# Performance work log

Hardware: AMD Instinct MI355X
Metric: run time of the kernel (lower is better)

The kernel has to match this reference:

```python
import jax, jax.numpy as jnp
import numpy as np

B, H, N, P = 2, 8, 2048, 64   # batch, heads, seq, head_dim
M, D = 4, 256                 # sketch count, sketch feature dim


def setup_inputs() -> dict:
    key = jax.random.key(0)
    kq, kk, ks, kr = jax.random.split(key, 4)
    scale = P ** -0.5  # keep exp(QK) numerically tame, std(dot) ~= 1/8
    Q = jax.random.normal(kq, (B, H, N, P), dtype=jnp.float32) * scale
    K = jax.random.normal(kk, (B, H, N, P), dtype=jnp.float32) * scale
    # indices into the concatenated [Q;K] token axis of length 2N
    sketching_matrix = jax.random.randint(ks, (B, M, D), 0, 2 * N)
    # Rademacher random signs, broadcast over [b,h,2n] in the reduction
    random_sign = jnp.sign(jax.random.normal(kr, (M, D), dtype=jnp.float32))
    random_sign = jnp.where(random_sign == 0, 1.0, random_sign)
    return {"Q": Q, "K": K, "sketching_matrix": sketching_matrix,
            "random_sign": random_sign}


def reference(Q, K, sketching_matrix, random_sign):
    b, h, n, p = Q.shape
    X = jnp.concatenate([Q, K], axis=2)          # [b,h,2n,p]
    Xt = jnp.transpose(X, (0, 2, 1, 3))          # [b,2n,h,p]
    # gather sketched landmarks: [b,m,d,h,p] -> [b,h,m,d,p]
    XS = Xt[jnp.arange(b)[:, None, None], sketching_matrix]
    XS = jnp.transpose(XS, (0, 3, 1, 2, 4))
    # RS_SM accumulate branch: exp of inner products, random-sign reduce over m
    product = jnp.einsum('bhnp,bhmdp->bhnmd', X, XS)   # [b,h,2n,m,d]
    AS = jnp.einsum('bhnmd,md->bhnd', jnp.exp(product), random_sign)
    return AS.astype(Q.dtype)                    # [b,h,2n,d]
```

## Files before the change

### kernel.cpp

```cpp
#include <hip/hip_runtime.h>
#include <hip/hip_bf16.h>

typedef __attribute__((ext_vector_type(8))) short short8;
typedef __attribute__((ext_vector_type(4))) float f32x4;

namespace {
constexpr int Nc  = 2048;
constexpr int NXc = 4096;
constexpr int Pc  = 64;
constexpr int Mc  = 4;
constexpr int Dc  = 256;
constexpr int BH  = 16;
constexpr int LDW = 72;
constexpr float LOG2E = 1.4426950408889634f;
}

__device__ inline float fexp2(float x) {
#if __has_builtin(__builtin_amdgcn_exp2f)
  return __builtin_amdgcn_exp2f(x);
#else
  return exp2f(x);
#endif
}

__device__ inline unsigned int bfpack(float a, float b) {
  union { __hip_bfloat162 h; unsigned int u; } cv;
  cv.h = __float22bfloat162_rn(make_float2(a, b));
  return cv.u;
}

__global__ __launch_bounds__(256) void prepass_kernel(
    const float* __restrict__ Q, const float* __restrict__ K,
    const int* __restrict__ SK, __hip_bfloat16* __restrict__ Wb)
{
  const int t  = blockIdx.x * 256 + threadIdx.x;
  const int q  = t & 7;
  const int r  = t >> 3;
  const int bh = r >> 10;
  const int md = r & 1023;
  const int b  = bh >> 3;
  const int idx = SK[b * (Mc * Dc) + md];
  const float* src = (idx < Nc) ? (Q + ((size_t)bh * Nc + idx) * Pc)
                                : (K + ((size_t)bh * Nc + (idx - Nc)) * Pc);
  const f32x4* s4 = (const f32x4*)(src + q * 8);
  f32x4 f0 = s4[0], f1 = s4[1];
  uint4 u;
  u.x = bfpack(f0.x * LOG2E, f0.y * LOG2E);
  u.y = bfpack(f0.z * LOG2E, f0.w * LOG2E);
  u.z = bfpack(f1.x * LOG2E, f1.y * LOG2E);
  u.w = bfpack(f1.z * LOG2E, f1.w * LOG2E);
  *(uint4*)(Wb + (size_t)r * Pc + q * 8) = u;
}

__global__ __launch_bounds__(256, 4) void sketch_main(
    const float* __restrict__ Q, const float* __restrict__ K,
    const __hip_bfloat16* __restrict__ Wb,
    const float* __restrict__ SGN, float* __restrict__ OUT)
{
  __shared__ __hip_bfloat16 Ws[2][64][LDW];
  __shared__ float Ss[Mc * Dc];

  const int t    = threadIdx.x;
  const int lane = t & 63;
  const int wv   = t >> 6;
  const int brow = lane & 15;
  const int q    = lane >> 4;
  const int bh   = blockIdx.y;
  const int n0   = blockIdx.x * 64;

  for (int i = t; i < Mc * Dc; i += 256) Ss[i] = SGN[i];

  const int nrow = n0 + wv * 16 + brow;
  const float* xsrc = (n0 < Nc) ? (Q + ((size_t)bh * Nc + nrow) * Pc)
                                : (K + ((size_t)bh * Nc + (nrow - Nc)) * Pc);
  f32x4 x0 = *(const f32x4*)(xsrc + q * 8);
  f32x4 x1 = *(const f32x4*)(xsrc + q * 8 + 4);
  f32x4 x2 = *(const f32x4*)(xsrc + 32 + q * 8);
  f32x4 x3 = *(const f32x4*)(xsrc + 32 + q * 8 + 4);
  short8 bfr0, bfr1;
  {
    union { short8 s; uint4 u; } c0, c1;
    c0.u.x = bfpack(x0.x, x0.y); c0.u.y = bfpack(x0.z, x0.w);
    c0.u.z = bfpack(x1.x, x1.y); c0.u.w = bfpack(x1.z, x1.w);
    c1.u.x = bfpack(x2.x, x2.y); c1.u.y = bfpack(x2.z, x2.w);
    c1.u.z = bfpack(x3.x, x3.y); c1.u.w = bfpack(x3.z, x3.w);
    bfr0 = c0.s; bfr1 = c1.s;
  }

  const __hip_bfloat16* wbase = Wb + (size_t)bh * (Mc * Dc) * Pc;
  const int tr = t >> 2;
  const int tq = t & 3;

  auto crow = [](int p) { return (p & 3) * Dc + (p >> 2) * 64; };

  {
    const __hip_bfloat16* wp = wbase + (size_t)(crow(0) + tr) * Pc + tq * 16;
    uint4 wa = *(const uint4*)wp;
    uint4 wb = *(const uint4*)(wp + 8);
    *(uint4*)&Ws[0][tr][tq * 16]     = wa;
    *(uint4*)&Ws[0][tr][tq * 16 + 8] = wb;
  }
  __syncthreads();

  f32x4 AS[4];
  #pragma unroll
  for (int dt = 0; dt < 4; ++dt) AS[dt] = (f32x4){0.f, 0.f, 0.f, 0.f};

  for (int p = 0; p < 16; ++p) {
    const int pn = (p < 15) ? p + 1 : 15;
    const __hip_bfloat16* wp = wbase + (size_t)(crow(pn) + tr) * Pc + tq * 16;
    uint4 wa = *(const uint4*)wp;
    uint4 wb = *(const uint4*)(wp + 8);

    const int buf = p & 1;
    const int m   = p & 3;
    const int dc  = p >> 2;

    #pragma unroll
    for (int dt = 0; dt < 4; ++dt) {
      short8 a0 = *(const short8*)&Ws[buf][dt * 16 + brow][q * 8];
      short8 a1 = *(const short8*)&Ws[buf][dt * 16 + brow][32 + q * 8];
      f32x4 c = {0.f, 0.f, 0.f, 0.f};
      c = __builtin_amdgcn_mfma_f32_16x16x32_bf16(a0, bfr0, c, 0, 0, 0);
      c = __builtin_amdgcn_mfma_f32_16x16x32_bf16(a1, bfr1, c, 0, 0, 0);
      const f32x4 sg = *(const f32x4*)&Ss[m * Dc + dc * 64 + dt * 16 + q * 4];
      AS[dt].x = fmaf(sg.x, fexp2(c.x), AS[dt].x);
      AS[dt].y = fmaf(sg.y, fexp2(c.y), AS[dt].y);
      AS[dt].z = fmaf(sg.z, fexp2(c.z), AS[dt].z);
      AS[dt].w = fmaf(sg.w, fexp2(c.w), AS[dt].w);
    }

    if (m == 3) {
      float* orow = OUT + ((size_t)bh * NXc + nrow) * Dc + dc * 64 + q * 4;
      #pragma unroll
      for (int dt = 0; dt < 4; ++dt) {
        *(f32x4*)(orow + dt * 16) = AS[dt];
        AS[dt] = (f32x4){0.f, 0.f, 0.f, 0.f};
      }
    }

    *(uint4*)&Ws[buf ^ 1][tr][tq * 16]     = wa;
    *(uint4*)&Ws[buf ^ 1][tr][tq * 16 + 8] = wb;
    __syncthreads();
  }
}

extern "C" void kernel_launch(void* const* d_in, const int* in_sizes, int n_in,
                              void* d_out, int out_size, void* d_ws, size_t ws_size,
                              hipStream_t stream) {
  (void)in_sizes; (void)n_in; (void)out_size; (void)ws_size;
  const float* Q   = (const float*)d_in[0];
  const float* K   = (const float*)d_in[1];
  const int*   SK  = (const int*)d_in[2];
  const float* SGN = (const float*)d_in[3];
  float* OUT = (float*)d_out;

  __hip_bfloat16* Wb = (__hip_bfloat16*)d_ws;

  prepass_kernel<<<dim3(512), dim3(256), 0, stream>>>(Q, K, SK, Wb);
  sketch_main<<<dim3(NXc / 64, BH), dim3(256), 0, stream>>>(Q, K, Wb, SGN, OUT);
}
```

Measured before the change: 102.2 us.

## Enlarge token tile to 128 and split sketch columns across waves

Each block now handles 128 tokens instead of 64. Each wave holds eight 16-token X fragments in registers and owns a fixed 16-column slice of the sketch landmarks. This reuses each LDS-loaded landmark fragment across eight MFMA tiles, cutting LDS reads and halving how often the shared landmark tile is reloaded from global memory per token. In exchange it raises register pressure (occupancy hint drops from 4 to 2 blocks), halves the number of blocks, and changes output stores to a strided row pattern.

```diff
diff --git a/kernel.cpp b/kernel.cpp
--- a/kernel.cpp
+++ b/kernel.cpp
@@ -11,6 +11,7 @@
 constexpr int Mc  = 4;
 constexpr int Dc  = 256;
 constexpr int BH  = 16;
+constexpr int TN  = 128;
 constexpr int LDW = 72;
 constexpr float LOG2E = 1.4426950408889634f;
 }
@@ -52,7 +53,7 @@
   *(uint4*)(Wb + (size_t)r * Pc + q * 8) = u;
 }
 
-__global__ __launch_bounds__(256, 4) void sketch_main(
+__global__ __launch_bounds__(256, 2) void sketch_main(
     const float* __restrict__ Q, const float* __restrict__ K,
     const __hip_bfloat16* __restrict__ Wb,
     const float* __restrict__ SGN, float* __restrict__ OUT)
@@ -66,25 +67,28 @@
   const int brow = lane & 15;
   const int q    = lane >> 4;
   const int bh   = blockIdx.y;
-  const int n0   = blockIdx.x * 64;
+  const int n0   = blockIdx.x * TN;
 
   for (int i = t; i < Mc * Dc; i += 256) Ss[i] = SGN[i];
 
-  const int nrow = n0 + wv * 16 + brow;
-  const float* xsrc = (n0 < Nc) ? (Q + ((size_t)bh * Nc + nrow) * Pc)
-                                : (K + ((size_t)bh * Nc + (nrow - Nc)) * Pc);
-  f32x4 x0 = *(const f32x4*)(xsrc + q * 8);
-  f32x4 x1 = *(const f32x4*)(xsrc + q * 8 + 4);
-  f32x4 x2 = *(const f32x4*)(xsrc + 32 + q * 8);
-  f32x4 x3 = *(const f32x4*)(xsrc + 32 + q * 8 + 4);
-  short8 bfr0, bfr1;
+  short8 bx[8][2];
   {
-    union { short8 s; uint4 u; } c0, c1;
-    c0.u.x = bfpack(x0.x, x0.y); c0.u.y = bfpack(x0.z, x0.w);
-    c0.u.z = bfpack(x1.x, x1.y); c0.u.w = bfpack(x1.z, x1.w);
-    c1.u.x = bfpack(x2.x, x2.y); c1.u.y = bfpack(x2.z, x2.w);
-    c1.u.z = bfpack(x3.x, x3.y); c1.u.w = bfpack(x3.z, x3.w);
-    bfr0 = c0.s; bfr1 = c1.s;
+    const float* xbase = (n0 < Nc) ? (Q + ((size_t)bh * Nc + n0) * Pc)
+                                   : (K + ((size_t)bh * Nc + (n0 - Nc)) * Pc);
+    #pragma unroll
+    for (int tj = 0; tj < 8; ++tj) {
+      const float* xr = xbase + (size_t)(tj * 16 + brow) * Pc + q * 8;
+      f32x4 f0 = *(const f32x4*)xr;
+      f32x4 f1 = *(const f32x4*)(xr + 4);
+      f32x4 f2 = *(const f32x4*)(xr + 32);
+      f32x4 f3 = *(const f32x4*)(xr + 36);
+      union { short8 s; uint4 u; } c0, c1;
+      c0.u.x = bfpack(f0.x, f0.y); c0.u.y = bfpack(f0.z, f0.w);
+      c0.u.z = bfpack(f1.x, f1.y); c0.u.w = bfpack(f1.z, f1.w);
+      c1.u.x = bfpack(f2.x, f2.y); c1.u.y = bfpack(f2.z, f2.w);
+      c1.u.z = bfpack(f3.x, f3.y); c1.u.w = bfpack(f3.z, f3.w);
+      bx[tj][0] = c0.s; bx[tj][1] = c1.s;
+    }
   }
 
   const __hip_bfloat16* wbase = Wb + (size_t)bh * (Mc * Dc) * Pc;
@@ -102,9 +106,9 @@
   }
   __syncthreads();
 
-  f32x4 AS[4];
+  f32x4 AS[8];
   #pragma unroll
-  for (int dt = 0; dt < 4; ++dt) AS[dt] = (f32x4){0.f, 0.f, 0.f, 0.f};
+  for (int tj = 0; tj < 8; ++tj) AS[tj] = (f32x4){0.f, 0.f, 0.f, 0.f};
 
   for (int p = 0; p < 16; ++p) {
     const int pn = (p < 15) ? p + 1 : 15;
@@ -116,26 +120,28 @@
     const int m   = p & 3;
     const int dc  = p >> 2;
 
+    short8 a0 = *(const short8*)&Ws[buf][wv * 16 + brow][q * 8];
+    short8 a1 = *(const short8*)&Ws[buf][wv * 16 + brow][32 + q * 8];
+
+    const f32x4 sg = *(const f32x4*)&Ss[m * Dc + dc * 64 + wv * 16 + q * 4];
+
     #pragma unroll
-    for (int dt = 0; dt < 4; ++dt) {
-      short8 a0 = *(const short8*)&Ws[buf][dt * 16 + brow][q * 8];
-      short8 a1 = *(const short8*)&Ws[buf][dt * 16 + brow][32 + q * 8];
+    for (int tj = 0; tj < 8; ++tj) {
       f32x4 c = {0.f, 0.f, 0.f, 0.f};
-      c = __builtin_amdgcn_mfma_f32_16x16x32_bf16(a0, bfr0, c, 0, 0, 0);
-      c = __builtin_amdgcn_mfma_f32_16x16x32_bf16(a1, bfr1, c, 0, 0, 0);
-      const f32x4 sg = *(const f32x4*)&Ss[m * Dc + dc * 64 + dt * 16 + q * 4];
-      AS[dt].x = fmaf(sg.x, fexp2(c.x), AS[dt].x);
-      AS[dt].y = fmaf(sg.y, fexp2(c.y), AS[dt].y);
-      AS[dt].z = fmaf(sg.z, fexp2(c.z), AS[dt].z);
-      AS[dt].w = fmaf(sg.w, fexp2(c.w), AS[dt].w);
+      c = __builtin_amdgcn_mfma_f32_16x16x32_bf16(a0, bx[tj][0], c, 0, 0, 0);
+      c = __builtin_amdgcn_mfma_f32_16x16x32_bf16(a1, bx[tj][1], c, 0, 0, 0);
+      AS[tj].x = fmaf(sg.x, fexp2(c.x), AS[tj].x);
+      AS[tj].y = fmaf(sg.y, fexp2(c.y), AS[tj].y);
+      AS[tj].z = fmaf(sg.z, fexp2(c.z), AS[tj].z);
+      AS[tj].w = fmaf(sg.w, fexp2(c.w), AS[tj].w);
     }
 
     if (m == 3) {
-      float* orow = OUT + ((size_t)bh * NXc + nrow) * Dc + dc * 64 + q * 4;
+      float* obase = OUT + ((size_t)bh * NXc + n0) * Dc + dc * 64 + wv * 16 + q * 4;
       #pragma unroll
-      for (int dt = 0; dt < 4; ++dt) {
-        *(f32x4*)(orow + dt * 16) = AS[dt];
-        AS[dt] = (f32x4){0.f, 0.f, 0.f, 0.f};
+      for (int tj = 0; tj < 8; ++tj) {
+        *(f32x4*)(obase + (size_t)(tj * 16 + brow) * Dc) = AS[tj];
+        AS[tj] = (f32x4){0.f, 0.f, 0.f, 0.f};
       }
     }
 
@@ -158,5 +164,5 @@
   __hip_bfloat16* Wb = (__hip_bfloat16*)d_ws;
 
   prepass_kernel<<<dim3(512), dim3(256), 0, stream>>>(Q, K, SK, Wb);
-  sketch_main<<<dim3(NXc / 64, BH), dim3(256), 0, stream>>>(Q, K, Wb, SGN, OUT);
+  sketch_main<<<dim3(NXc / TN, BH), dim3(256), 0, stream>>>(Q, K, Wb, SGN, OUT);
 }
```

After: 105.7 us. 3.4% more time.
